# Performance work log

Measured on AMD Instinct MI355X. Metric: run time of the kernel, lower is better.

Reference implementation:

```python
import jax, jax.numpy as jnp
import numpy as np

N = 50000
E = 800000
D_IN = 64
D_OUT = 64


def setup_inputs() -> dict:
    key = jax.random.key(0)
    k_x, k_e, k_ws, k_bs, k_wn, k_bn = jax.random.split(key, 6)
    x = jax.random.normal(k_x, (N, D_IN), dtype=jnp.float32)
    edge_index = jax.random.randint(k_e, (2, E), 0, N, dtype=jnp.int64)
    # nn.Linear params: weight [out, in], bias [out]
    lim = 1.0 / np.sqrt(D_IN)
    W_self = jax.random.uniform(k_ws, (D_OUT, D_IN), minval=-lim, maxval=lim, dtype=jnp.float32)
    b_self = jax.random.uniform(k_bs, (D_OUT,), minval=-lim, maxval=lim, dtype=jnp.float32)
    W_neigh = jax.random.uniform(k_wn, (D_OUT, D_IN), minval=-lim, maxval=lim, dtype=jnp.float32)
    b_neigh = jax.random.uniform(k_bn, (D_OUT,), minval=-lim, maxval=lim, dtype=jnp.float32)
    return {"x": x, "edge_index": edge_index, "W_self": W_self, "b_self": b_self,
            "W_neigh": W_neigh, "b_neigh": b_neigh}


def reference(x, edge_index, W_self, b_self, W_neigh, b_neigh):
    row, col = edge_index[0], edge_index[1]
    n = x.shape[0]
    # degree of each destination node (clamped to 1)
    deg = jax.ops.segment_sum(jnp.ones_like(row, dtype=x.dtype), row, num_segments=n)
    deg = jnp.maximum(deg, 1.0)
    # mean-aggregate neighbor features: scatter-add x[col] into row buckets
    agg = jax.ops.segment_sum(x[col], row, num_segments=n)  # [N, D_IN]
    agg = agg / deg[:, None]
    out = x @ W_self.T + b_self + agg @ W_neigh.T + b_neigh
    return out
```

## Files before the change

### kernel.cpp

```cpp
#include <hip/hip_runtime.h>
#include <hip/hip_bf16.h>


#define D    64
#define CAP  64
#define TPB  256
#define TPW  16
#define WPT  2
#define TPBL 2
#define EPT  8
#define CAPB 4608

typedef __attribute__((ext_vector_type(8))) short bf16x8;
typedef __attribute__((ext_vector_type(4))) float f32x4;

__device__ __forceinline__ unsigned short f2bf(float f) {
    unsigned u = __float_as_uint(f);
    return (unsigned short)((u + 0x7fffu + ((u >> 16) & 1u)) >> 16);
}
__device__ __forceinline__ float bf2f(unsigned short s) {
    return __uint_as_float((unsigned)s << 16);
}

__device__ __forceinline__ int load_idx(const void* ei, int use64, long long pos) {
    if (use64) return (int)((const long long*)ei)[pos];
    return ((const int*)ei)[pos];
}

__global__ __launch_bounds__(256) void bin_k(
        const float* __restrict__ x, const void* __restrict__ ei,
        unsigned* __restrict__ staging, unsigned* __restrict__ gcur,
        unsigned short* __restrict__ xb, int N, int E, int NBr) {
    __shared__ unsigned lcnt[256];
    __shared__ unsigned lbase[256];
    __shared__ int s_use64;
    const int t = threadIdx.x;
    lcnt[t] = 0u;
    if (t < 64) {
        long long v = (t < 16) ? ((const long long*)ei)[t] : 0;
        unsigned long long bad = __ballot(t < 16 && (v < 0 || v >= (long long)N));
        if (t == 0) s_use64 = (bad == 0ULL) ? 1 : 0;
    }
    __syncthreads();
    const int use64 = s_use64;
    const int e0 = blockIdx.x * (256 * EPT);
    unsigned pk[EPT], lp[EPT];
    int bk[EPT];
    #pragma unroll
    for (int j = 0; j < EPT; ++j) {
        int e = e0 + j * 256 + t;
        if (e < E) {
            int r = load_idx(ei, use64, e);
            int c = load_idx(ei, use64, (long long)E + e);
            pk[j] = ((unsigned)r << 16) | (unsigned)(c & 0xffff);
            bk[j] = r >> 8;
            lp[j] = atomicAdd(&lcnt[bk[j]], 1u);
        } else bk[j] = -1;
    }
    __syncthreads();
    if (t < NBr) {
        unsigned n = lcnt[t];
        lbase[t] = n ? atomicAdd(&gcur[t], n) : 0u;
    }
    __syncthreads();
    #pragma unroll
    for (int j = 0; j < EPT; ++j) {
        if (bk[j] >= 0) {
            unsigned p = lbase[bk[j]] + lp[j];
            if (p < CAPB) staging[(unsigned)bk[j] * CAPB + p] = pk[j];
        }
    }
    int tid = blockIdx.x * 256 + t;
    int NT  = gridDim.x * 256;
    int NV  = (N * D) >> 2;
    for (int i = tid; i < NV; i += NT) {
        float4 v = *(const float4*)&x[i * 4];
        ushort4 o;
        o.x = f2bf(v.x); o.y = f2bf(v.y); o.z = f2bf(v.z); o.w = f2bf(v.w);
        *(ushort4*)&xb[i * 4] = o;
    }
}

__global__ __launch_bounds__(256) void bucket_k(
        const unsigned* __restrict__ staging, const unsigned* __restrict__ gcur,
        int* __restrict__ cnt, unsigned short* __restrict__ slots, int N) {
    __shared__ unsigned short sl[256 * CAP];
    __shared__ unsigned scnt[256];
    const int t = threadIdx.x, b = blockIdx.x;
    scnt[t] = 0u;
    __syncthreads();
    unsigned nb = gcur[b]; if (nb > CAPB) nb = CAPB;
    for (unsigned e = t; e < nb; e += 256) {
        unsigned pk = staging[(unsigned)b * CAPB + e];
        unsigned rl = (pk >> 16) & 255u;
        unsigned pos = atomicAdd(&scnt[rl], 1u);
        if (pos < CAP) sl[(rl << 6) + pos] = (unsigned short)(pk & 0xffffu);
    }
    __syncthreads();
    int n0 = b << 8;
    int nn = N - n0; if (nn > 256) nn = 256;
    const uint4* s4 = (const uint4*)sl;
    uint4* g4 = (uint4*)&slots[(size_t)n0 * CAP];
    for (int i = t; i < nn * 8; i += 256) g4[i] = s4[i];
    if (t < nn) cnt[n0 + t] = (int)scnt[t];
}

__global__ __launch_bounds__(TPB) void fused_k(
        const unsigned short* __restrict__ xb,
        const int* __restrict__ cnt, const unsigned short* __restrict__ slots,
        const float* __restrict__ Ws, const float* __restrict__ bs,
        const float* __restrict__ Wn, const float* __restrict__ bn,
        float* __restrict__ out, int N) {
    __shared__ __align__(16) short wcat[D][136];
    __shared__ __align__(16) short mtile[TPBL][TPW][72];

    const int t = threadIdx.x;
    for (int i = t; i < D * 128; i += TPB) {
        int f = i >> 7, kk = i & 127;
        float v = (kk < D) ? Ws[f * D + kk] : Wn[f * D + (kk - D)];
        wcat[f][kk] = (short)f2bf(v);
    }
    __syncthreads();

    const int w    = t >> 6;
    const int lane = t & 63;
    const int m_   = lane & 15;
    const int quad = lane >> 4;
    const int ql   = m_;
    const int q4   = quad;
    const int pair = w >> 1;
    const int half = w & 1;

    const int tile = (blockIdx.x * TPBL + pair) * TPW;

    #pragma unroll
    for (int pp = 0; pp < 2; ++pp) {
        int p = half * 2 + pp;
        int n = tile + p * 4 + q4;
        int deg = (n < N) ? cnt[n] : 0;
        int mm = deg < CAP ? deg : CAP;
        float4 s = make_float4(0.f, 0.f, 0.f, 0.f);
        for (int base = 0; base < mm; base += 16) {
            int sv = (base + ql < mm) ? (int)slots[n * CAP + base + ql] : 0;
            int mq = mm - base; if (mq > 16) mq = 16;
            unsigned off[16];
            #pragma unroll
            for (int j = 0; j < 16; ++j) {
                int c = __shfl(sv, (q4 << 4) + j);
                off[j] = (unsigned)c * D + 4 * ql;
            }
            ushort4 v[16];
            #pragma unroll
            for (int j = 0; j < 16; ++j)
                v[j] = *(const ushort4*)&xb[off[j]];
            #pragma unroll
            for (int j = 0; j < 16; ++j) {
                float m = (j < mq) ? 1.0f : 0.0f;
                s.x = fmaf(m, bf2f(v[j].x), s.x);
                s.y = fmaf(m, bf2f(v[j].y), s.y);
                s.z = fmaf(m, bf2f(v[j].z), s.z);
                s.w = fmaf(m, bf2f(v[j].w), s.w);
            }
        }
        float dinv = (deg > 0) ? 1.0f / (float)deg : 0.0f;
        short4 mv;
        mv.x = (short)f2bf(s.x * dinv); mv.y = (short)f2bf(s.y * dinv);
        mv.z = (short)f2bf(s.z * dinv); mv.w = (short)f2bf(s.w * dinv);
        *(short4*)&mtile[pair][p * 4 + q4][4 * ql] = mv;
    }
    __syncthreads();

    int nrow = tile + m_;
    const unsigned short* xr = xb + (size_t)(nrow < N ? nrow : 0) * D;
    bf16x8 afrag[4];
    afrag[0] = *(const bf16x8*)&xr[quad * 8];
    afrag[1] = *(const bf16x8*)&xr[32 + quad * 8];
    #pragma unroll
    for (int ks = 2; ks < 4; ++ks)
        afrag[ks] = *(const bf16x8*)&mtile[pair][m_][(ks - 2) * 32 + quad * 8];

    f32x4 acc[2];
    #pragma unroll
    for (int i = 0; i < 2; ++i) {
        int fcol = (half * 2 + i) * 16 + m_;
        float bsum = bs[fcol] + bn[fcol];
        acc[i] = (f32x4){bsum, bsum, bsum, bsum};
    }
    #pragma unroll
    for (int i = 0; i < 2; ++i) {
        int nf = half * 2 + i;
        #pragma unroll
        for (int ks = 0; ks < 4; ++ks) {
            bf16x8 bfr = *(const bf16x8*)&wcat[nf * 16 + m_][ks * 32 + quad * 8];
            acc[i] = __builtin_amdgcn_mfma_f32_16x16x32_bf16(
                afrag[ks], bfr, acc[i], 0, 0, 0);
        }
    }

    #pragma unroll
    for (int i = 0; i < 2; ++i) {
        int fcol = (half * 2 + i) * 16 + m_;
        #pragma unroll
        for (int r = 0; r < 4; ++r) {
            int node = tile + quad * 4 + r;
            if (node < N) out[(size_t)node * D + fcol] = acc[i][r];
        }
    }
}

extern "C" void kernel_launch(void* const* d_in, const int* in_sizes, int n_in,
                              void* d_out, int out_size, void* d_ws, size_t ws_size,
                              hipStream_t stream) {
    const float* x  = (const float*)d_in[0];
    const void*  ei = d_in[1];
    const float* Ws = (const float*)d_in[2];
    const float* bs = (const float*)d_in[3];
    const float* Wn = (const float*)d_in[4];
    const float* bn = (const float*)d_in[5];
    float* out = (float*)d_out;

    int N = in_sizes[0] / D;
    int E = in_sizes[1] / 2;

    unsigned short* xb    = (unsigned short*)d_ws;
    unsigned short* slots = xb + (size_t)N * D;
    int*            cnt   = (int*)(slots + (size_t)N * CAP);

    int NBr = (N + 255) >> 8;
    unsigned* staging = (unsigned*)d_out;
    unsigned* gcur    = staging + (size_t)NBr * CAPB;

    hipMemsetAsync(gcur, 0, (size_t)NBr * sizeof(unsigned), stream);

    int binb = (E + 256 * EPT - 1) / (256 * EPT);
    bin_k<<<binb, 256, 0, stream>>>(x, ei, staging, gcur, xb, N, E, NBr);

    bucket_k<<<NBr, 256, 0, stream>>>(staging, gcur, cnt, slots, N);

    int ntiles  = (N + TPW - 1) / TPW;
    int fblocks = (ntiles + TPBL - 1) / TPBL;
    fused_k<<<fblocks, TPB, 0, stream>>>(xb, cnt, slots, Ws, bs, Wn, bn, out, N);
}
```

Measured before the change: 126.1 us.

## Fuse memset, binning, bucketing and SAGE kernels into one cooperative persistent kernel

Replaces the memset and three separate kernel launches with a single cooperative kernel. It uses grid-wide syncs between the phases and grid-stride loops, with a shared-memory union reused across phases. The aim is to remove launch overhead and inter-kernel gaps. In exchange, the grid is limited to the occupancy-bound resident size, and the large shared-memory union (bucket phase ~33KB) lowers occupancy for the gather phase. Grid syncs also add barrier cost.

New measurement: 238.3 us. 89.0% more time.

```diff
diff --git a/kernel.cpp b/kernel.cpp
--- a/kernel.cpp
+++ b/kernel.cpp
@@ -1,14 +1,16 @@
 #include <hip/hip_runtime.h>
 #include <hip/hip_bf16.h>
+#include <hip/hip_cooperative_groups.h>
+
+namespace cg = cooperative_groups;
 
 
 #define D    64
 #define CAP  64
-#define TPB  256
 #define TPW  16
-#define WPT  2
 #define TPBL 2
 #define EPT  8
+#define CHUNK (256 * EPT)
 #define CAPB 4608
 
 typedef __attribute__((ext_vector_type(8))) short bf16x8;
@@ -21,21 +23,34 @@
 __device__ __forceinline__ float bf2f(unsigned short s) {
     return __uint_as_float((unsigned)s << 16);
 }
-
 __device__ __forceinline__ int load_idx(const void* ei, int use64, long long pos) {
     if (use64) return (int)((const long long*)ei)[pos];
     return ((const int*)ei)[pos];
 }
 
-__global__ __launch_bounds__(256) void bin_k(
+union __align__(16) ShUnion {
+    struct { unsigned lcnt[256]; unsigned lbase[256]; } bin;
+    struct { unsigned scnt[256]; unsigned short sl[256 * CAP]; } bkt;
+    struct { short wcat[D][136]; short mtile[TPBL][TPW][72]; } fz;
+};
+
+__global__ __launch_bounds__(256) void all_k(
         const float* __restrict__ x, const void* __restrict__ ei,
         unsigned* __restrict__ staging, unsigned* __restrict__ gcur,
-        unsigned short* __restrict__ xb, int N, int E, int NBr) {
-    __shared__ unsigned lcnt[256];
-    __shared__ unsigned lbase[256];
+        unsigned short* __restrict__ xb, int* __restrict__ cnt,
+        unsigned short* __restrict__ slots,
+        const float* __restrict__ Ws, const float* __restrict__ bs,
+        const float* __restrict__ Wn, const float* __restrict__ bn,
+        float* __restrict__ out, int N, int E, int NBr) {
+    cg::grid_group grid = cg::this_grid();
+    __shared__ ShUnion sh;
     __shared__ int s_use64;
     const int t = threadIdx.x;
-    lcnt[t] = 0u;
+
+    if (blockIdx.x == 0)
+        for (int i = t; i < NBr; i += 256) gcur[i] = 0u;
+    grid.sync();
+
     if (t < 64) {
         long long v = (t < 16) ? ((const long long*)ei)[t] : 0;
         unsigned long long bad = __ballot(t < 16 && (v < 0 || v >= (long long)N));
@@ -43,82 +58,77 @@
     }
     __syncthreads();
     const int use64 = s_use64;
-    const int e0 = blockIdx.x * (256 * EPT);
-    unsigned pk[EPT], lp[EPT];
-    int bk[EPT];
-    #pragma unroll
-    for (int j = 0; j < EPT; ++j) {
-        int e = e0 + j * 256 + t;
-        if (e < E) {
-            int r = load_idx(ei, use64, e);
-            int c = load_idx(ei, use64, (long long)E + e);
-            pk[j] = ((unsigned)r << 16) | (unsigned)(c & 0xffff);
-            bk[j] = r >> 8;
-            lp[j] = atomicAdd(&lcnt[bk[j]], 1u);
-        } else bk[j] = -1;
-    }
-    __syncthreads();
-    if (t < NBr) {
-        unsigned n = lcnt[t];
-        lbase[t] = n ? atomicAdd(&gcur[t], n) : 0u;
-    }
-    __syncthreads();
-    #pragma unroll
-    for (int j = 0; j < EPT; ++j) {
-        if (bk[j] >= 0) {
-            unsigned p = lbase[bk[j]] + lp[j];
-            if (p < CAPB) staging[(unsigned)bk[j] * CAPB + p] = pk[j];
-        }
-    }
-    int tid = blockIdx.x * 256 + t;
-    int NT  = gridDim.x * 256;
-    int NV  = (N * D) >> 2;
-    for (int i = tid; i < NV; i += NT) {
-        float4 v = *(const float4*)&x[i * 4];
-        ushort4 o;
-        o.x = f2bf(v.x); o.y = f2bf(v.y); o.z = f2bf(v.z); o.w = f2bf(v.w);
-        *(ushort4*)&xb[i * 4] = o;
-    }
-}
-
-__global__ __launch_bounds__(256) void bucket_k(
-        const unsigned* __restrict__ staging, const unsigned* __restrict__ gcur,
-        int* __restrict__ cnt, unsigned short* __restrict__ slots, int N) {
-    __shared__ unsigned short sl[256 * CAP];
-    __shared__ unsigned scnt[256];
-    const int t = threadIdx.x, b = blockIdx.x;
-    scnt[t] = 0u;
-    __syncthreads();
-    unsigned nb = gcur[b]; if (nb > CAPB) nb = CAPB;
-    for (unsigned e = t; e < nb; e += 256) {
-        unsigned pk = staging[(unsigned)b * CAPB + e];
-        unsigned rl = (pk >> 16) & 255u;
-        unsigned pos = atomicAdd(&scnt[rl], 1u);
-        if (pos < CAP) sl[(rl << 6) + pos] = (unsigned short)(pk & 0xffffu);
-    }
-    __syncthreads();
-    int n0 = b << 8;
-    int nn = N - n0; if (nn > 256) nn = 256;
-    const uint4* s4 = (const uint4*)sl;
-    uint4* g4 = (uint4*)&slots[(size_t)n0 * CAP];
-    for (int i = t; i < nn * 8; i += 256) g4[i] = s4[i];
-    if (t < nn) cnt[n0 + t] = (int)scnt[t];
-}
-
-__global__ __launch_bounds__(TPB) void fused_k(
-        const unsigned short* __restrict__ xb,
-        const int* __restrict__ cnt, const unsigned short* __restrict__ slots,
-        const float* __restrict__ Ws, const float* __restrict__ bs,
-        const float* __restrict__ Wn, const float* __restrict__ bn,
-        float* __restrict__ out, int N) {
-    __shared__ __align__(16) short wcat[D][136];
-    __shared__ __align__(16) short mtile[TPBL][TPW][72];
-
-    const int t = threadIdx.x;
-    for (int i = t; i < D * 128; i += TPB) {
+    const int nchunks = (E + CHUNK - 1) / CHUNK;
+    for (int ch = blockIdx.x; ch < nchunks; ch += gridDim.x) {
+        sh.bin.lcnt[t] = 0u;
+        __syncthreads();
+        const int e0 = ch * CHUNK;
+        unsigned pk[EPT], lp[EPT];
+        int bk[EPT];
+        #pragma unroll
+        for (int j = 0; j < EPT; ++j) {
+            int e = e0 + j * 256 + t;
+            if (e < E) {
+                int r = load_idx(ei, use64, e);
+                int c = load_idx(ei, use64, (long long)E + e);
+                pk[j] = ((unsigned)r << 16) | (unsigned)(c & 0xffff);
+                bk[j] = r >> 8;
+                lp[j] = atomicAdd(&sh.bin.lcnt[bk[j]], 1u);
+            } else bk[j] = -1;
+        }
+        __syncthreads();
+        if (t < NBr) {
+            unsigned n = sh.bin.lcnt[t];
+            sh.bin.lbase[t] = n ? atomicAdd(&gcur[t], n) : 0u;
+        }
+        __syncthreads();
+        #pragma unroll
+        for (int j = 0; j < EPT; ++j) {
+            if (bk[j] >= 0) {
+                unsigned p = sh.bin.lbase[bk[j]] + lp[j];
+                if (p < CAPB) staging[(unsigned)bk[j] * CAPB + p] = pk[j];
+            }
+        }
+        __syncthreads();
+    }
+    {
+        int tid = blockIdx.x * 256 + t;
+        int NT  = gridDim.x * 256;
+        int NV  = (N * D) >> 2;
+        for (int i = tid; i < NV; i += NT) {
+            float4 v = *(const float4*)&x[i * 4];
+            ushort4 o;
+            o.x = f2bf(v.x); o.y = f2bf(v.y); o.z = f2bf(v.z); o.w = f2bf(v.w);
+            *(ushort4*)&xb[i * 4] = o;
+        }
+    }
+    grid.sync();
+
+    for (int b = blockIdx.x; b < NBr; b += gridDim.x) {
+        sh.bkt.scnt[t] = 0u;
+        __syncthreads();
+        unsigned nb = gcur[b]; if (nb > CAPB) nb = CAPB;
+        for (unsigned e = t; e < nb; e += 256) {
+            unsigned pk = staging[(unsigned)b * CAPB + e];
+            unsigned rl = (pk >> 16) & 255u;
+            unsigned pos = atomicAdd(&sh.bkt.scnt[rl], 1u);
+            if (pos < CAP) sh.bkt.sl[(rl << 6) + pos] = (unsigned short)(pk & 0xffffu);
+        }
+        __syncthreads();
+        int n0 = b << 8;
+        int nn = N - n0; if (nn > 256) nn = 256;
+        const uint4* s4 = (const uint4*)sh.bkt.sl;
+        uint4* g4 = (uint4*)&slots[(size_t)n0 * CAP];
+        for (int i = t; i < nn * 8; i += 256) g4[i] = s4[i];
+        if (t < nn) cnt[n0 + t] = (int)sh.bkt.scnt[t];
+        __syncthreads();
+    }
+    grid.sync();
+
+    for (int i = t; i < D * 128; i += 256) {
         int f = i >> 7, kk = i & 127;
         float v = (kk < D) ? Ws[f * D + kk] : Wn[f * D + (kk - D)];
-        wcat[f][kk] = (short)f2bf(v);
+        sh.fz.wcat[f][kk] = (short)f2bf(v);
     }
     __syncthreads();
 
@@ -130,81 +140,86 @@
     const int q4   = quad;
     const int pair = w >> 1;
     const int half = w & 1;
-
-    const int tile = (blockIdx.x * TPBL + pair) * TPW;
-
-    #pragma unroll
-    for (int pp = 0; pp < 2; ++pp) {
-        int p = half * 2 + pp;
-        int n = tile + p * 4 + q4;
-        int deg = (n < N) ? cnt[n] : 0;
-        int mm = deg < CAP ? deg : CAP;
-        float4 s = make_float4(0.f, 0.f, 0.f, 0.f);
-        for (int base = 0; base < mm; base += 16) {
-            int sv = (base + ql < mm) ? (int)slots[n * CAP + base + ql] : 0;
-            int mq = mm - base; if (mq > 16) mq = 16;
-            unsigned off[16];
+    const int ntiles = (N + TPW - 1) / TPW;
+    const int nbt = (ntiles + TPBL - 1) / TPBL;
+
+    for (int bt = blockIdx.x; bt < nbt; bt += gridDim.x) {
+        const int tile = (bt * TPBL + pair) * TPW;
+
+        #pragma unroll
+        for (int pp = 0; pp < 2; ++pp) {
+            int p = half * 2 + pp;
+            int n = tile + p * 4 + q4;
+            int deg = (n < N) ? cnt[n] : 0;
+            int mm = deg < CAP ? deg : CAP;
+            float4 s = make_float4(0.f, 0.f, 0.f, 0.f);
+            for (int base = 0; base < mm; base += 16) {
+                int sv = (base + ql < mm) ? (int)slots[n * CAP + base + ql] : 0;
+                int mq = mm - base; if (mq > 16) mq = 16;
+                unsigned off[16];
+                #pragma unroll
+                for (int j = 0; j < 16; ++j) {
+                    int c = __shfl(sv, (q4 << 4) + j);
+                    off[j] = (unsigned)c * D + 4 * ql;
+                }
+                ushort4 v[16];
+                #pragma unroll
+                for (int j = 0; j < 16; ++j)
+                    v[j] = *(const ushort4*)&xb[off[j]];
+                #pragma unroll
+                for (int j = 0; j < 16; ++j) {
+                    float m = (j < mq) ? 1.0f : 0.0f;
+                    s.x = fmaf(m, bf2f(v[j].x), s.x);
+                    s.y = fmaf(m, bf2f(v[j].y), s.y);
+                    s.z = fmaf(m, bf2f(v[j].z), s.z);
+                    s.w = fmaf(m, bf2f(v[j].w), s.w);
+                }
+            }
+            float dinv = (deg > 0) ? 1.0f / (float)deg : 0.0f;
+            short4 mv;
+            mv.x = (short)f2bf(s.x * dinv); mv.y = (short)f2bf(s.y * dinv);
+            mv.z = (short)f2bf(s.z * dinv); mv.w = (short)f2bf(s.w * dinv);
+            *(short4*)&sh.fz.mtile[pair][p * 4 + q4][4 * ql] = mv;
+        }
+        __syncthreads();
+
+        int nrow = tile + m_;
+        const unsigned short* xr = xb + (size_t)(nrow < N ? nrow : 0) * D;
+        bf16x8 afrag[4];
+        afrag[0] = *(const bf16x8*)&xr[quad * 8];
+        afrag[1] = *(const bf16x8*)&xr[32 + quad * 8];
+        #pragma unroll
+        for (int ks = 2; ks < 4; ++ks)
+            afrag[ks] = *(const bf16x8*)&sh.fz.mtile[pair][m_][(ks - 2) * 32 + quad * 8];
+
+        f32x4 acc[2];
+        #pragma unroll
+        for (int i = 0; i < 2; ++i) {
+            int fcol = (half * 2 + i) * 16 + m_;
+            float bsum = bs[fcol] + bn[fcol];
+            acc[i] = (f32x4){bsum, bsum, bsum, bsum};
+        }
+        #pragma unroll
+        for (int i = 0; i < 2; ++i) {
+            int nf = half * 2 + i;
             #pragma unroll
-            for (int j = 0; j < 16; ++j) {
-                int c = __shfl(sv, (q4 << 4) + j);
-                off[j] = (unsigned)c * D + 4 * ql;
-            }
-            ushort4 v[16];
+            for (int ks = 0; ks < 4; ++ks) {
+                bf16x8 bfr = *(const bf16x8*)&sh.fz.wcat[nf * 16 + m_][ks * 32 + quad * 8];
+                acc[i] = __builtin_amdgcn_mfma_f32_16x16x32_bf16(
+                    afrag[ks], bfr, acc[i], 0, 0, 0);
+            }
+        }
+
+        #pragma unroll
+        for (int i = 0; i < 2; ++i) {
+            int fcol = (half * 2 + i) * 16 + m_;
             #pragma unroll
-            for (int j = 0; j < 16; ++j)
-                v[j] = *(const ushort4*)&xb[off[j]];
-            #pragma unroll
-            for (int j = 0; j < 16; ++j) {
-                float m = (j < mq) ? 1.0f : 0.0f;
-                s.x = fmaf(m, bf2f(v[j].x), s.x);
-                s.y = fmaf(m, bf2f(v[j].y), s.y);
-                s.z = fmaf(m, bf2f(v[j].z), s.z);
-                s.w = fmaf(m, bf2f(v[j].w), s.w);
-            }
-        }
-        float dinv = (deg > 0) ? 1.0f / (float)deg : 0.0f;
-        short4 mv;
-        mv.x = (short)f2bf(s.x * dinv); mv.y = (short)f2bf(s.y * dinv);
-        mv.z = (short)f2bf(s.z * dinv); mv.w = (short)f2bf(s.w * dinv);
-        *(short4*)&mtile[pair][p * 4 + q4][4 * ql] = mv;
-    }
-    __syncthreads();
-
-    int nrow = tile + m_;
-    const unsigned short* xr = xb + (size_t)(nrow < N ? nrow : 0) * D;
-    bf16x8 afrag[4];
-    afrag[0] = *(const bf16x8*)&xr[quad * 8];
-    afrag[1] = *(const bf16x8*)&xr[32 + quad * 8];
-    #pragma unroll
-    for (int ks = 2; ks < 4; ++ks)
-        afrag[ks] = *(const bf16x8*)&mtile[pair][m_][(ks - 2) * 32 + quad * 8];
-
-    f32x4 acc[2];
-    #pragma unroll
-    for (int i = 0; i < 2; ++i) {
-        int fcol = (half * 2 + i) * 16 + m_;
-        float bsum = bs[fcol] + bn[fcol];
-        acc[i] = (f32x4){bsum, bsum, bsum, bsum};
-    }
-    #pragma unroll
-    for (int i = 0; i < 2; ++i) {
-        int nf = half * 2 + i;
-        #pragma unroll
-        for (int ks = 0; ks < 4; ++ks) {
-            bf16x8 bfr = *(const bf16x8*)&wcat[nf * 16 + m_][ks * 32 + quad * 8];
-            acc[i] = __builtin_amdgcn_mfma_f32_16x16x32_bf16(
-                afrag[ks], bfr, acc[i], 0, 0, 0);
-        }
-    }
-
-    #pragma unroll
-    for (int i = 0; i < 2; ++i) {
-        int fcol = (half * 2 + i) * 16 + m_;
-        #pragma unroll
-        for (int r = 0; r < 4; ++r) {
-            int node = tile + quad * 4 + r;
-            if (node < N) out[(size_t)node * D + fcol] = acc[i][r];
-        }
+            for (int r = 0; r < 4; ++r) {
+                int node = tile + quad * 4 + r;
+                if (node < N) out[(size_t)node * D + fcol] = acc[i][r];
+            }
+        }
+        __syncthreads();
     }
 }
 
@@ -230,14 +245,24 @@
     unsigned* staging = (unsigned*)d_out;
     unsigned* gcur    = staging + (size_t)NBr * CAPB;
 
-    hipMemsetAsync(gcur, 0, (size_t)NBr * sizeof(unsigned), stream);
-
-    int binb = (E + 256 * EPT - 1) / (256 * EPT);
-    bin_k<<<binb, 256, 0, stream>>>(x, ei, staging, gcur, xb, N, E, NBr);
-
-    bucket_k<<<NBr, 256, 0, stream>>>(staging, gcur, cnt, slots, N);
-
-    int ntiles  = (N + TPW - 1) / TPW;
-    int fblocks = (ntiles + TPBL - 1) / TPBL;
-    fused_k<<<fblocks, TPB, 0, stream>>>(xb, cnt, slots, Ws, bs, Wn, bn, out, N);
-}
+    static int coop_grid = 0;
+    if (coop_grid == 0) {
+        int occ = 0, ncu = 0, dev = 0;
+        (void)hipGetDevice(&dev);
+        (void)hipOccupancyMaxActiveBlocksPerMultiprocessor(&occ, all_k, 256, 0);
+        (void)hipDeviceGetAttribute(&ncu, hipDeviceAttributeMultiprocessorCount, dev);
+        if (occ < 1) occ = 1;
+        if (ncu < 1) ncu = 256;
+        coop_grid = occ * ncu;
+        int ntiles = (N + TPW - 1) / TPW;
+        int nbt = (ntiles + TPBL - 1) / TPBL;
+        if (coop_grid > nbt) coop_grid = nbt;
+    }
+
+    void* args[] = { (void*)&x, (void*)&ei, (void*)&staging, (void*)&gcur,
+                     (void*)&xb, (void*)&cnt, (void*)&slots,
+                     (void*)&Ws, (void*)&bs, (void*)&Wn, (void*)&bn,
+                     (void*)&out, (void*)&N, (void*)&E, (void*)&NBr };
+    (void)hipLaunchCooperativeKernel(all_k, dim3(coop_grid), dim3(256),
+                                     args, 0, stream);
+}
```

## Fuse bucket sort into aggregation kernel, bucketing in shared memory per block

Applied to the files above, without the earlier changes.

Removes the separate bucket kernel and its global slots/cnt arrays. Each aggregation block of 64 nodes now scans its 256-node staging bucket and builds per-node neighbor lists in shared memory, then aggregates and runs the MFMA projection over two 32-node iterations. This drops one launch and a global write/read of the slot table. In exchange, each staging bucket is read four times (once per sub-block), and staging moves from the output buffer to the workspace.

Result: slower. 133.2 us (+5.6%).

```diff
diff --git a/kernel.cpp b/kernel.cpp
--- a/kernel.cpp
+++ b/kernel.cpp
@@ -4,10 +4,9 @@
 
 #define D    64
 #define CAP  64
-#define TPB  256
 #define TPW  16
-#define WPT  2
-#define TPBL 2
+#define BKN  64
+#define SLP  66
 #define EPT  8
 #define CAPB 4608
 
@@ -21,7 +20,6 @@
 __device__ __forceinline__ float bf2f(unsigned short s) {
     return __uint_as_float((unsigned)s << 16);
 }
-
 __device__ __forceinline__ int load_idx(const void* ei, int use64, long long pos) {
     if (use64) return (int)((const long long*)ei)[pos];
     return ((const int*)ei)[pos];
@@ -81,44 +79,37 @@
     }
 }
 
-__global__ __launch_bounds__(256) void bucket_k(
+__global__ __launch_bounds__(256) void fuse2_k(
+        const unsigned short* __restrict__ xb,
         const unsigned* __restrict__ staging, const unsigned* __restrict__ gcur,
-        int* __restrict__ cnt, unsigned short* __restrict__ slots, int N) {
-    __shared__ unsigned short sl[256 * CAP];
-    __shared__ unsigned scnt[256];
-    const int t = threadIdx.x, b = blockIdx.x;
-    scnt[t] = 0u;
-    __syncthreads();
-    unsigned nb = gcur[b]; if (nb > CAPB) nb = CAPB;
-    for (unsigned e = t; e < nb; e += 256) {
-        unsigned pk = staging[(unsigned)b * CAPB + e];
-        unsigned rl = (pk >> 16) & 255u;
-        unsigned pos = atomicAdd(&scnt[rl], 1u);
-        if (pos < CAP) sl[(rl << 6) + pos] = (unsigned short)(pk & 0xffffu);
-    }
-    __syncthreads();
-    int n0 = b << 8;
-    int nn = N - n0; if (nn > 256) nn = 256;
-    const uint4* s4 = (const uint4*)sl;
-    uint4* g4 = (uint4*)&slots[(size_t)n0 * CAP];
-    for (int i = t; i < nn * 8; i += 256) g4[i] = s4[i];
-    if (t < nn) cnt[n0 + t] = (int)scnt[t];
-}
-
-__global__ __launch_bounds__(TPB) void fused_k(
-        const unsigned short* __restrict__ xb,
-        const int* __restrict__ cnt, const unsigned short* __restrict__ slots,
         const float* __restrict__ Ws, const float* __restrict__ bs,
         const float* __restrict__ Wn, const float* __restrict__ bn,
         float* __restrict__ out, int N) {
     __shared__ __align__(16) short wcat[D][136];
-    __shared__ __align__(16) short mtile[TPBL][TPW][72];
+    __shared__ __align__(16) short mtile[2][TPW][72];
+    __shared__ unsigned short sl[BKN * SLP];
+    __shared__ unsigned scnt[BKN];
 
     const int t = threadIdx.x;
-    for (int i = t; i < D * 128; i += TPB) {
+    for (int i = t; i < D * 128; i += 256) {
         int f = i >> 7, kk = i & 127;
         float v = (kk < D) ? Ws[f * D + kk] : Wn[f * D + (kk - D)];
         wcat[f][kk] = (short)f2bf(v);
+    }
+    if (t < BKN) scnt[t] = 0u;
+    __syncthreads();
+
+    const int node0 = blockIdx.x * BKN;
+    const int q = blockIdx.x >> 2;
+    unsigned nstg = gcur[q]; if (nstg > CAPB) nstg = CAPB;
+    const unsigned* sbase = staging + (size_t)q * CAPB;
+    for (unsigned e = t; e < nstg; e += 256) {
+        unsigned pk = sbase[e];
+        int local = (int)(pk >> 16) - node0;
+        if ((unsigned)local < (unsigned)BKN) {
+            unsigned pos = atomicAdd(&scnt[local], 1u);
+            if (pos < CAP) sl[local * SLP + pos] = (unsigned short)(pk & 0xffffu);
+        }
     }
     __syncthreads();
 
@@ -131,80 +122,84 @@
     const int pair = w >> 1;
     const int half = w & 1;
 
-    const int tile = (blockIdx.x * TPBL + pair) * TPW;
-
-    #pragma unroll
-    for (int pp = 0; pp < 2; ++pp) {
-        int p = half * 2 + pp;
-        int n = tile + p * 4 + q4;
-        int deg = (n < N) ? cnt[n] : 0;
-        int mm = deg < CAP ? deg : CAP;
-        float4 s = make_float4(0.f, 0.f, 0.f, 0.f);
-        for (int base = 0; base < mm; base += 16) {
-            int sv = (base + ql < mm) ? (int)slots[n * CAP + base + ql] : 0;
-            int mq = mm - base; if (mq > 16) mq = 16;
-            unsigned off[16];
+    for (int it = 0; it < 2; ++it) {
+        const int tile = node0 + (it * 2 + pair) * TPW;
+
+        #pragma unroll
+        for (int pp = 0; pp < 2; ++pp) {
+            int p = half * 2 + pp;
+            int n = tile + p * 4 + q4;
+            int nl = n - node0;
+            int deg = (n < N) ? (int)scnt[nl] : 0;
+            int mm = deg < CAP ? deg : CAP;
+            float4 s = make_float4(0.f, 0.f, 0.f, 0.f);
+            for (int seg = 0; seg < mm; seg += 16) {
+                int sv = (seg + ql < mm) ? (int)sl[nl * SLP + seg + ql] : 0;
+                int mq = mm - seg; if (mq > 16) mq = 16;
+                unsigned off[16];
+                #pragma unroll
+                for (int j = 0; j < 16; ++j) {
+                    int c = __shfl(sv, (q4 << 4) + j);
+                    off[j] = (unsigned)c * D + 4 * ql;
+                }
+                ushort4 v[16];
+                #pragma unroll
+                for (int j = 0; j < 16; ++j)
+                    v[j] = *(const ushort4*)&xb[off[j]];
+                #pragma unroll
+                for (int j = 0; j < 16; ++j) {
+                    float m = (j < mq) ? 1.0f : 0.0f;
+                    s.x = fmaf(m, bf2f(v[j].x), s.x);
+                    s.y = fmaf(m, bf2f(v[j].y), s.y);
+                    s.z = fmaf(m, bf2f(v[j].z), s.z);
+                    s.w = fmaf(m, bf2f(v[j].w), s.w);
+                }
+            }
+            float dinv = (deg > 0) ? 1.0f / (float)deg : 0.0f;
+            short4 mv;
+            mv.x = (short)f2bf(s.x * dinv); mv.y = (short)f2bf(s.y * dinv);
+            mv.z = (short)f2bf(s.z * dinv); mv.w = (short)f2bf(s.w * dinv);
+            *(short4*)&mtile[pair][p * 4 + q4][4 * ql] = mv;
+        }
+        __syncthreads();
+
+        int nrow = tile + m_;
+        const unsigned short* xr = xb + (size_t)(nrow < N ? nrow : 0) * D;
+        bf16x8 afrag[4];
+        afrag[0] = *(const bf16x8*)&xr[quad * 8];
+        afrag[1] = *(const bf16x8*)&xr[32 + quad * 8];
+        #pragma unroll
+        for (int ks = 2; ks < 4; ++ks)
+            afrag[ks] = *(const bf16x8*)&mtile[pair][m_][(ks - 2) * 32 + quad * 8];
+
+        f32x4 acc[2];
+        #pragma unroll
+        for (int i = 0; i < 2; ++i) {
+            int fcol = (half * 2 + i) * 16 + m_;
+            float bsum = bs[fcol] + bn[fcol];
+            acc[i] = (f32x4){bsum, bsum, bsum, bsum};
+        }
+        #pragma unroll
+        for (int i = 0; i < 2; ++i) {
+            int nf = half * 2 + i;
             #pragma unroll
-            for (int j = 0; j < 16; ++j) {
-                int c = __shfl(sv, (q4 << 4) + j);
-                off[j] = (unsigned)c * D + 4 * ql;
+            for (int ks = 0; ks < 4; ++ks) {
+                bf16x8 bfr = *(const bf16x8*)&wcat[nf * 16 + m_][ks * 32 + quad * 8];
+                acc[i] = __builtin_amdgcn_mfma_f32_16x16x32_bf16(
+                    afrag[ks], bfr, acc[i], 0, 0, 0);
             }
-            ushort4 v[16];
+        }
+
+        #pragma unroll
+        for (int i = 0; i < 2; ++i) {
+            int fcol = (half * 2 + i) * 16 + m_;
             #pragma unroll
-            for (int j = 0; j < 16; ++j)
-                v[j] = *(const ushort4*)&xb[off[j]];
-            #pragma unroll
-            for (int j = 0; j < 16; ++j) {
-                float m = (j < mq) ? 1.0f : 0.0f;
-                s.x = fmaf(m, bf2f(v[j].x), s.x);
-                s.y = fmaf(m, bf2f(v[j].y), s.y);
-                s.z = fmaf(m, bf2f(v[j].z), s.z);
-                s.w = fmaf(m, bf2f(v[j].w), s.w);
+            for (int r = 0; r < 4; ++r) {
+                int node = tile + quad * 4 + r;
+                if (node < N) out[(size_t)node * D + fcol] = acc[i][r];
             }
         }
-        float dinv = (deg > 0) ? 1.0f / (float)deg : 0.0f;
-        short4 mv;
-        mv.x = (short)f2bf(s.x * dinv); mv.y = (short)f2bf(s.y * dinv);
-        mv.z = (short)f2bf(s.z * dinv); mv.w = (short)f2bf(s.w * dinv);
-        *(short4*)&mtile[pair][p * 4 + q4][4 * ql] = mv;
-    }
-    __syncthreads();
-
-    int nrow = tile + m_;
-    const unsigned short* xr = xb + (size_t)(nrow < N ? nrow : 0) * D;
-    bf16x8 afrag[4];
-    afrag[0] = *(const bf16x8*)&xr[quad * 8];
-    afrag[1] = *(const bf16x8*)&xr[32 + quad * 8];
-    #pragma unroll
-    for (int ks = 2; ks < 4; ++ks)
-        afrag[ks] = *(const bf16x8*)&mtile[pair][m_][(ks - 2) * 32 + quad * 8];
-
-    f32x4 acc[2];
-    #pragma unroll
-    for (int i = 0; i < 2; ++i) {
-        int fcol = (half * 2 + i) * 16 + m_;
-        float bsum = bs[fcol] + bn[fcol];
-        acc[i] = (f32x4){bsum, bsum, bsum, bsum};
-    }
-    #pragma unroll
-    for (int i = 0; i < 2; ++i) {
-        int nf = half * 2 + i;
-        #pragma unroll
-        for (int ks = 0; ks < 4; ++ks) {
-            bf16x8 bfr = *(const bf16x8*)&wcat[nf * 16 + m_][ks * 32 + quad * 8];
-            acc[i] = __builtin_amdgcn_mfma_f32_16x16x32_bf16(
-                afrag[ks], bfr, acc[i], 0, 0, 0);
-        }
-    }
-
-    #pragma unroll
-    for (int i = 0; i < 2; ++i) {
-        int fcol = (half * 2 + i) * 16 + m_;
-        #pragma unroll
-        for (int r = 0; r < 4; ++r) {
-            int node = tile + quad * 4 + r;
-            if (node < N) out[(size_t)node * D + fcol] = acc[i][r];
-        }
+        __syncthreads();
     }
 }
 
@@ -222,22 +217,17 @@
     int N = in_sizes[0] / D;
     int E = in_sizes[1] / 2;
 
-    unsigned short* xb    = (unsigned short*)d_ws;
-    unsigned short* slots = xb + (size_t)N * D;
-    int*            cnt   = (int*)(slots + (size_t)N * CAP);
-
     int NBr = (N + 255) >> 8;
-    unsigned* staging = (unsigned*)d_out;
-    unsigned* gcur    = staging + (size_t)NBr * CAPB;
+    unsigned short* xb      = (unsigned short*)d_ws;
+    unsigned*       staging = (unsigned*)(xb + (size_t)N * D);
+    unsigned*       gcur    = staging + (size_t)NBr * CAPB;
 
     hipMemsetAsync(gcur, 0, (size_t)NBr * sizeof(unsigned), stream);
 
     int binb = (E + 256 * EPT - 1) / (256 * EPT);
     bin_k<<<binb, 256, 0, stream>>>(x, ei, staging, gcur, xb, N, E, NBr);
 
-    bucket_k<<<NBr, 256, 0, stream>>>(staging, gcur, cnt, slots, N);
-
-    int ntiles  = (N + TPW - 1) / TPW;
-    int fblocks = (ntiles + TPBL - 1) / TPBL;
-    fused_k<<<fblocks, TPB, 0, stream>>>(xb, cnt, slots, Ws, bs, Wn, bn, out, N);
-}
+    int fblocks = (N + BKN - 1) / BKN;
+    fuse2_k<<<fblocks, 256, 0, stream>>>(xb, staging, gcur,
+                                         Ws, bs, Wn, bn, out, N);
+}
```
